# Kernel tuning notes

Measured on AMD Instinct MI355X. Metric: run time of the kernel, lower is better.

## Reference

```python
import jax, jax.numpy as jnp
import numpy as np

N = 1_048_576   # collocation points
D_IN = 3        # seq_net[0]
H = 32          # hidden width (seq_net[1..3])
B = 4           # seq_net[-1] = number of parallel branches / outputs


def setup_inputs() -> dict:
    key = jax.random.key(0)
    ks = jax.random.split(key, 9)

    def init_w(k, shape, fan_in):
        bound = 1.0 / np.sqrt(fan_in)
        return jax.random.uniform(k, shape, jnp.float32, -bound, bound)

    x = jax.random.normal(ks[0], (N, D_IN), dtype=jnp.float32)
    # Per-branch weights stacked on leading branch axis B (torch.nn.Linear init ranges).
    W0 = init_w(ks[1], (B, D_IN, H), D_IN)
    b0 = init_w(ks[2], (B, H), D_IN)
    W1 = init_w(ks[3], (B, H, H), H)
    b1 = init_w(ks[4], (B, H), H)
    W2 = init_w(ks[5], (B, H, H), H)
    b2 = init_w(ks[6], (B, H), H)
    W3 = init_w(ks[7], (B, H, 1), H)
    b3 = init_w(ks[8], (B, 1), H)
    return {"x": x, "W0": W0, "b0": b0, "W1": W1, "b1": b1,
            "W2": W2, "b2": b2, "W3": W3, "b3": b3}


def reference(x, W0, b0, W1, b1, W2, b2, W3, b3):
    # All B branches computed as one batched GEMM chain (same math as the
    # python loop over per-branch Linear+tanh stacks in PFNN.forward).
    h = jnp.tanh(jnp.einsum('nd,bdh->bnh', x, W0) + b0[:, None, :])   # [B,N,H]
    h = jnp.tanh(jnp.einsum('bnd,bdh->bnh', h, W1) + b1[:, None, :])  # [B,N,H]
    h = jnp.tanh(jnp.einsum('bnd,bdh->bnh', h, W2) + b2[:, None, :])  # [B,N,H]
    out = jnp.einsum('bnd,bdh->bnh', h, W3) + b3[:, None, :]          # [B,N,1]
    # torch.cat(preds, dim=1): branch outputs side by side -> [N, B]
    return jnp.transpose(out[:, :, 0])
```

## Files before the change

### kernel.cpp

```cpp
#include <hip/hip_runtime.h>


#define NPTS 1048576
#define BLOCK 256
#define HROW 80
#define SCALE 2.8853900817779268f

#define OFF_BSC  16384
#define OFF_W0F  17408
#define OFF_B0P  25600
#define OFF_W3P  26112

using f16   = _Float16;
using f16x8 = __attribute__((ext_vector_type(8))) _Float16;
using f32x4 = __attribute__((ext_vector_type(4))) float;
using hfx2  = decltype(__builtin_amdgcn_cvt_pkrtz(0.0f, 0.0f));

__device__ __forceinline__ void inv4c(float v0, float v1, float v2, float v3,
                                      float& o0, float& o1, float& o2, float& o3)
{
    float a0 = __builtin_amdgcn_exp2f(v0) + 1.0f;
    float a1 = __builtin_amdgcn_exp2f(v1) + 1.0f;
    float a2 = __builtin_amdgcn_exp2f(v2) + 1.0f;
    float a3 = __builtin_amdgcn_exp2f(v3) + 1.0f;
    float p01 = a0 * a1;
    float p23 = a2 * a3;
    float p   = p01 * p23;
    float r   = __builtin_amdgcn_rcpf(p);
    float r01 = r * p23;
    float r23 = r * p01;
    o0 = __builtin_fmaf(r01, a1, -0.5f);
    o1 = __builtin_fmaf(r01, a0, -0.5f);
    o2 = __builtin_fmaf(r23, a3, -0.5f);
    o3 = __builtin_fmaf(r23, a2, -0.5f);
}

__device__ __forceinline__ void epi_mt(const f32x4& c0, const f32x4& c1, int mt,
                                       unsigned char* __restrict__ H,
                                       int col, int quad)
{
    #pragma unroll
    for (int r = 0; r < 4; r += 2) {
        int p = mt * 16 + quad * 4 + r;
        float o0, o1, o2, o3;
        inv4c(c0[r], c1[r], c0[r + 1], c1[r + 1], o0, o1, o2, o3);
        union { hfx2 h; unsigned int u; } cv0, cv1;
        cv0.h = __builtin_amdgcn_cvt_pkrtz(o0, o1);
        cv1.h = __builtin_amdgcn_cvt_pkrtz(o2, o3);
        *reinterpret_cast<unsigned int*>(H + p * HROW + 4 * col)       = cv0.u;
        *reinterpret_cast<unsigned int*>(H + (p + 1) * HROW + 4 * col) = cv1.u;
    }
}

__global__ void prep_kernel(const float* __restrict__ W0, const float* __restrict__ b0,
                            const float* __restrict__ W1, const float* __restrict__ b1,
                            const float* __restrict__ W2, const float* __restrict__ b2,
                            const float* __restrict__ W3,
                            unsigned char* __restrict__ ws)
{
    int i = blockIdx.x * 256 + threadIdx.x;
    if (i < 8192) {
        int k = i & 31, n = (i >> 5) & 15, t = (i >> 9) & 1, b = (i >> 10) & 3, l = i >> 12;
        int f = 2 * n + t;
        const float* W = l ? W2 : W1;
        reinterpret_cast<f16*>(ws)[i] = (f16)(-2.0f * SCALE * W[(b * 32 + k) * 32 + f]);
    } else if (i < 8448) {
        int j = i - 8192;
        int n = j & 15, t = (j >> 4) & 1, b = (j >> 5) & 3, l = j >> 7;
        const float* bb = l ? b2 : b1;
        reinterpret_cast<float*>(ws + OFF_BSC)[(((l * 4 + b) * 16 + n) << 1) | t]
            = SCALE * bb[b * 32 + 2 * n + t];
    } else if (i < 12544) {
        int j = i - 8448;
        int k = j & 31, n = (j >> 5) & 15, t = (j >> 9) & 1, b = (j >> 10) & 3;
        int f = 2 * n + t;
        int q = k >> 3, jj = k & 7;
        int row = -1; bool lo = false;
        if (q == 0 && jj < 6)      row = (jj < 3) ? jj : jj - 3;
        else if (q == 1 && jj < 3) { row = jj; lo = true; }
        f16 outv = (f16)0.0f;
        if (row >= 0) {
            float w  = SCALE * W0[(b * 3 + row) * 32 + f];
            f16   wh = (f16)w;
            outv = lo ? (f16)(w - (float)wh) : wh;
        }
        reinterpret_cast<f16*>(ws + OFF_W0F)[((b * 2 + t) * 16 + n) * 32 + k] = outv;
    } else if (i < 12672) {
        int j = i - 12544;
        int n = j & 15, t = (j >> 4) & 1, b = j >> 5;
        reinterpret_cast<float*>(ws + OFF_B0P)[(((b) * 16 + n) << 1) | t]
            = SCALE * b0[b * 32 + 2 * n + t];
    } else if (i < 12736) {
        int j = i - 12672;
        union { hfx2 h; unsigned int u; } cv;
        cv.h = __builtin_amdgcn_cvt_pkrtz(-2.0f * W3[2 * j], -2.0f * W3[2 * j + 1]);
        reinterpret_cast<unsigned int*>(ws + OFF_W3P)[j] = cv.u;
    }
}

__global__ __launch_bounds__(BLOCK, 8) void pfnn_kernel(
    const float* __restrict__ x, const unsigned char* __restrict__ ws,
    const float* __restrict__ b3,
    float* __restrict__ out)
{
    __shared__ __align__(16) unsigned char Hl[4][64 * HROW];

    const f16*   Wf  = reinterpret_cast<const f16*>(ws);
    const float* Bsc = reinterpret_cast<const float*>(ws + OFF_BSC);
    const f16*   W0f = reinterpret_cast<const f16*>(ws + OFF_W0F);
    const float* B0p = reinterpret_cast<const float*>(ws + OFF_B0P);
    const unsigned int* W3p = reinterpret_cast<const unsigned int*>(ws + OFF_W3P);

    const int t    = threadIdx.x;
    const int lane = t & 63;
    const int wv   = t >> 6;
    const int col  = lane & 15;
    const int quad = lane >> 4;
    unsigned char* __restrict__ H = &Hl[wv][0];

    const int n0 = blockIdx.x * BLOCK + t;
    const float x0 = x[3 * n0 + 0];
    const float x1 = x[3 * n0 + 1];
    const float x2 = x[3 * n0 + 2];

    f16x8 xfrag[4];
    {
        union { hfx2 h; int u; } q0_, q1_, q2_;
        q0_.h = __builtin_amdgcn_cvt_pkrtz(x0, x1);
        float r0 = x0 - (float)q0_.h[0];
        float r1 = x1 - (float)q0_.h[1];
        q1_.h = __builtin_amdgcn_cvt_pkrtz(x2, r0);
        float r2 = x2 - (float)q1_.h[0];
        q2_.h = __builtin_amdgcn_cvt_pkrtz(r1, r2);
        int d0 = q0_.u, d1 = q1_.u, d2 = q2_.u;
        #pragma unroll
        for (int mt = 0; mt < 4; ++mt) {
            int addr = 4 * (mt * 16 + col);
            union { int i[4]; f16x8 f; } u;
            u.i[0] = __builtin_amdgcn_ds_bpermute(addr, d0);
            u.i[1] = __builtin_amdgcn_ds_bpermute(addr, d1);
            u.i[2] = __builtin_amdgcn_ds_bpermute(addr, d2);
            u.i[3] = 0;
            xfrag[mt] = u.f;
        }
    }

    float res[4];

    #pragma unroll 2
    for (int b = 0; b < 4; ++b) {
        {
            const f16* wb = W0f + (b * 2) * 512;
            f16x8 bf0 = *reinterpret_cast<const f16x8*>(wb + col * 32 + quad * 8);
            f16x8 bf1 = *reinterpret_cast<const f16x8*>(wb + 512 + col * 32 + quad * 8);
            const float2 bp = *reinterpret_cast<const float2*>(B0p + ((b * 16 + col) << 1));
            f32x4 ci0 = {bp.x, bp.x, bp.x, bp.x};
            f32x4 ci1 = {bp.y, bp.y, bp.y, bp.y};

            #pragma unroll
            for (int mt = 0; mt < 4; ++mt) {
                f32x4 c0 = __builtin_amdgcn_mfma_f32_16x16x32_f16(xfrag[mt], bf0, ci0, 0, 0, 0);
                f32x4 c1 = __builtin_amdgcn_mfma_f32_16x16x32_f16(xfrag[mt], bf1, ci1, 0, 0, 0);
                epi_mt(c0, c1, mt, H, col, quad);
            }
        }

        #pragma unroll
        for (int l = 0; l < 2; ++l) {
            const f16* wb = Wf + ((l * 4 + b) * 2) * 512;
            f16x8 bf0 = *reinterpret_cast<const f16x8*>(wb + col * 32 + quad * 8);
            f16x8 bf1 = *reinterpret_cast<const f16x8*>(wb + 512 + col * 32 + quad * 8);
            const float2 bp = *reinterpret_cast<const float2*>(
                Bsc + (((l * 4 + b) * 16 + col) << 1));
            f32x4 ci0 = {bp.x, bp.x, bp.x, bp.x};
            f32x4 ci1 = {bp.y, bp.y, bp.y, bp.y};

            #pragma unroll
            for (int mt = 0; mt < 4; ++mt) {
                const f16x8 av = *reinterpret_cast<const f16x8*>(
                    H + (mt * 16 + col) * HROW + quad * 16);
                f32x4 c0 = __builtin_amdgcn_mfma_f32_16x16x32_f16(av, bf0, ci0, 0, 0, 0);
                f32x4 c1 = __builtin_amdgcn_mfma_f32_16x16x32_f16(av, bf1, ci1, 0, 0, 0);
                epi_mt(c0, c1, mt, H, col, quad);
            }
        }

        {
            float o = b3[b];
            const unsigned char* row = H + lane * HROW;
            const unsigned int* w3p = W3p + b * 16;
            #pragma unroll
            for (int i = 0; i < 4; ++i) {
                uint4 u = *reinterpret_cast<const uint4*>(row + 16 * i);
#if __has_builtin(__builtin_amdgcn_fdot2)
                union { unsigned int uu; hfx2 hh; } h0, h1, h2, h3, w0, w1, w2, w3u;
                h0.uu = u.x; h1.uu = u.y; h2.uu = u.z; h3.uu = u.w;
                w0.uu = w3p[4 * i];     w1.uu = w3p[4 * i + 1];
                w2.uu = w3p[4 * i + 2]; w3u.uu = w3p[4 * i + 3];
                o = __builtin_amdgcn_fdot2(h0.hh, w0.hh, o, false);
                o = __builtin_amdgcn_fdot2(h1.hh, w1.hh, o, false);
                o = __builtin_amdgcn_fdot2(h2.hh, w2.hh, o, false);
                o = __builtin_amdgcn_fdot2(h3.hh, w3u.hh, o, false);
#else
                union { unsigned int uu; f16 h[2]; } hh[4], wwu[4];
                hh[0].uu = u.x; hh[1].uu = u.y; hh[2].uu = u.z; hh[3].uu = u.w;
                #pragma unroll
                for (int q = 0; q < 4; ++q) {
                    wwu[q].uu = w3p[4 * i + q];
                    o = __builtin_fmaf((float)hh[q].h[0], (float)wwu[q].h[0], o);
                    o = __builtin_fmaf((float)hh[q].h[1], (float)wwu[q].h[1], o);
                }
#endif
            }
            res[b] = o;
        }
    }

    float4 r4 = make_float4(res[0], res[1], res[2], res[3]);
    *reinterpret_cast<float4*>(out + 4 * n0) = r4;
}

extern "C" void kernel_launch(void* const* d_in, const int* in_sizes, int n_in,
                              void* d_out, int out_size, void* d_ws, size_t ws_size,
                              hipStream_t stream) {
    const float* x  = (const float*)d_in[0];
    const float* W0 = (const float*)d_in[1];
    const float* b0 = (const float*)d_in[2];
    const float* W1 = (const float*)d_in[3];
    const float* b1 = (const float*)d_in[4];
    const float* W2 = (const float*)d_in[5];
    const float* b2 = (const float*)d_in[6];
    const float* W3 = (const float*)d_in[7];
    const float* b3 = (const float*)d_in[8];
    float* out = (float*)d_out;
    unsigned char* ws = (unsigned char*)d_ws;

    prep_kernel<<<dim3(50), dim3(256), 0, stream>>>(W0, b0, W1, b1, W2, b2, W3, ws);
    pfnn_kernel<<<dim3(NPTS / BLOCK), dim3(BLOCK), 0, stream>>>(x, ws, b3, out);
}
```

Measured before the change: 161.6 us.

## Software-pipeline branch loop: overlap next layer0 with final dot product

Restructures the per-branch loop so the last layer's H rows are read into registers, then the next branch's first-layer MFMA runs before the final dot products are computed. The dot product is split into four independent accumulators so it is less serialized. The loop is no longer unrolled, which is meant to cut code size and register pressure. The tradeoff is that holding the H rows live across layer0 costs extra registers, and the changed summation order alters rounding slightly.

```diff
diff --git a/kernel.cpp b/kernel.cpp
--- a/kernel.cpp
+++ b/kernel.cpp
@@ -50,6 +50,76 @@
         *reinterpret_cast<unsigned int*>(H + p * HROW + 4 * col)       = cv0.u;
         *reinterpret_cast<unsigned int*>(H + (p + 1) * HROW + 4 * col) = cv1.u;
     }
+}
+
+__device__ __forceinline__ void layer0_block(int b, const f16x8 (&xfrag)[4],
+                                             const f16* __restrict__ W0f,
+                                             const float* __restrict__ B0p,
+                                             unsigned char* __restrict__ H,
+                                             int col, int quad)
+{
+    const f16* wb = W0f + (b * 2) * 512;
+    f16x8 bf0 = *reinterpret_cast<const f16x8*>(wb + col * 32 + quad * 8);
+    f16x8 bf1 = *reinterpret_cast<const f16x8*>(wb + 512 + col * 32 + quad * 8);
+    const float2 bp = *reinterpret_cast<const float2*>(B0p + ((b * 16 + col) << 1));
+    f32x4 ci0 = {bp.x, bp.x, bp.x, bp.x};
+    f32x4 ci1 = {bp.y, bp.y, bp.y, bp.y};
+
+    #pragma unroll
+    for (int mt = 0; mt < 4; ++mt) {
+        f32x4 c0 = __builtin_amdgcn_mfma_f32_16x16x32_f16(xfrag[mt], bf0, ci0, 0, 0, 0);
+        f32x4 c1 = __builtin_amdgcn_mfma_f32_16x16x32_f16(xfrag[mt], bf1, ci1, 0, 0, 0);
+        epi_mt(c0, c1, mt, H, col, quad);
+    }
+}
+
+__device__ __forceinline__ void hidden_block(int l, int b,
+                                             const f16* __restrict__ Wf,
+                                             const float* __restrict__ Bsc,
+                                             unsigned char* __restrict__ H,
+                                             int col, int quad)
+{
+    const f16* wb = Wf + ((l * 4 + b) * 2) * 512;
+    f16x8 bf0 = *reinterpret_cast<const f16x8*>(wb + col * 32 + quad * 8);
+    f16x8 bf1 = *reinterpret_cast<const f16x8*>(wb + 512 + col * 32 + quad * 8);
+    const float2 bp = *reinterpret_cast<const float2*>(
+        Bsc + (((l * 4 + b) * 16 + col) << 1));
+    f32x4 ci0 = {bp.x, bp.x, bp.x, bp.x};
+    f32x4 ci1 = {bp.y, bp.y, bp.y, bp.y};
+
+    #pragma unroll
+    for (int mt = 0; mt < 4; ++mt) {
+        const f16x8 av = *reinterpret_cast<const f16x8*>(
+            H + (mt * 16 + col) * HROW + quad * 16);
+        f32x4 c0 = __builtin_amdgcn_mfma_f32_16x16x32_f16(av, bf0, ci0, 0, 0, 0);
+        f32x4 c1 = __builtin_amdgcn_mfma_f32_16x16x32_f16(av, bf1, ci1, 0, 0, 0);
+        epi_mt(c0, c1, mt, H, col, quad);
+    }
+}
+
+__device__ __forceinline__ float dot8(unsigned int ux, unsigned int uy,
+                                      unsigned int uz, unsigned int uw,
+                                      uint4 w, float acc)
+{
+#if __has_builtin(__builtin_amdgcn_fdot2)
+    union { unsigned int uu; hfx2 hh; } a0, a1, a2, a3, b0, b1, b2, b3;
+    a0.uu = ux; a1.uu = uy; a2.uu = uz; a3.uu = uw;
+    b0.uu = w.x; b1.uu = w.y; b2.uu = w.z; b3.uu = w.w;
+    acc = __builtin_amdgcn_fdot2(a0.hh, b0.hh, acc, false);
+    acc = __builtin_amdgcn_fdot2(a1.hh, b1.hh, acc, false);
+    acc = __builtin_amdgcn_fdot2(a2.hh, b2.hh, acc, false);
+    acc = __builtin_amdgcn_fdot2(a3.hh, b3.hh, acc, false);
+#else
+    union { unsigned int uu; f16 h[2]; } a[4], bw[4];
+    a[0].uu = ux; a[1].uu = uy; a[2].uu = uz; a[3].uu = uw;
+    bw[0].uu = w.x; bw[1].uu = w.y; bw[2].uu = w.z; bw[3].uu = w.w;
+    #pragma unroll
+    for (int q = 0; q < 4; ++q) {
+        acc = __builtin_fmaf((float)a[q].h[0], (float)bw[q].h[0], acc);
+        acc = __builtin_fmaf((float)a[q].h[1], (float)bw[q].h[1], acc);
+    }
+#endif
+    return acc;
 }
 
 __global__ void prep_kernel(const float* __restrict__ W0, const float* __restrict__ b0,
@@ -146,74 +216,45 @@
     }
 
     float res[4];
-
-    #pragma unroll 2
-    for (int b = 0; b < 4; ++b) {
-        {
-            const f16* wb = W0f + (b * 2) * 512;
-            f16x8 bf0 = *reinterpret_cast<const f16x8*>(wb + col * 32 + quad * 8);
-            f16x8 bf1 = *reinterpret_cast<const f16x8*>(wb + 512 + col * 32 + quad * 8);
-            const float2 bp = *reinterpret_cast<const float2*>(B0p + ((b * 16 + col) << 1));
-            f32x4 ci0 = {bp.x, bp.x, bp.x, bp.x};
-            f32x4 ci1 = {bp.y, bp.y, bp.y, bp.y};
-
-            #pragma unroll
-            for (int mt = 0; mt < 4; ++mt) {
-                f32x4 c0 = __builtin_amdgcn_mfma_f32_16x16x32_f16(xfrag[mt], bf0, ci0, 0, 0, 0);
-                f32x4 c1 = __builtin_amdgcn_mfma_f32_16x16x32_f16(xfrag[mt], bf1, ci1, 0, 0, 0);
-                epi_mt(c0, c1, mt, H, col, quad);
-            }
-        }
-
-        #pragma unroll
-        for (int l = 0; l < 2; ++l) {
-            const f16* wb = Wf + ((l * 4 + b) * 2) * 512;
-            f16x8 bf0 = *reinterpret_cast<const f16x8*>(wb + col * 32 + quad * 8);
-            f16x8 bf1 = *reinterpret_cast<const f16x8*>(wb + 512 + col * 32 + quad * 8);
-            const float2 bp = *reinterpret_cast<const float2*>(
-                Bsc + (((l * 4 + b) * 16 + col) << 1));
-            f32x4 ci0 = {bp.x, bp.x, bp.x, bp.x};
-            f32x4 ci1 = {bp.y, bp.y, bp.y, bp.y};
-
-            #pragma unroll
-            for (int mt = 0; mt < 4; ++mt) {
-                const f16x8 av = *reinterpret_cast<const f16x8*>(
-                    H + (mt * 16 + col) * HROW + quad * 16);
-                f32x4 c0 = __builtin_amdgcn_mfma_f32_16x16x32_f16(av, bf0, ci0, 0, 0, 0);
-                f32x4 c1 = __builtin_amdgcn_mfma_f32_16x16x32_f16(av, bf1, ci1, 0, 0, 0);
-                epi_mt(c0, c1, mt, H, col, quad);
-            }
-        }
-
-        {
-            float o = b3[b];
-            const unsigned char* row = H + lane * HROW;
-            const unsigned int* w3p = W3p + b * 16;
-            #pragma unroll
-            for (int i = 0; i < 4; ++i) {
-                uint4 u = *reinterpret_cast<const uint4*>(row + 16 * i);
-#if __has_builtin(__builtin_amdgcn_fdot2)
-                union { unsigned int uu; hfx2 hh; } h0, h1, h2, h3, w0, w1, w2, w3u;
-                h0.uu = u.x; h1.uu = u.y; h2.uu = u.z; h3.uu = u.w;
-                w0.uu = w3p[4 * i];     w1.uu = w3p[4 * i + 1];
-                w2.uu = w3p[4 * i + 2]; w3u.uu = w3p[4 * i + 3];
-                o = __builtin_amdgcn_fdot2(h0.hh, w0.hh, o, false);
-                o = __builtin_amdgcn_fdot2(h1.hh, w1.hh, o, false);
-                o = __builtin_amdgcn_fdot2(h2.hh, w2.hh, o, false);
-                o = __builtin_amdgcn_fdot2(h3.hh, w3u.hh, o, false);
-#else
-                union { unsigned int uu; f16 h[2]; } hh[4], wwu[4];
-                hh[0].uu = u.x; hh[1].uu = u.y; hh[2].uu = u.z; hh[3].uu = u.w;
-                #pragma unroll
-                for (int q = 0; q < 4; ++q) {
-                    wwu[q].uu = w3p[4 * i + q];
-                    o = __builtin_fmaf((float)hh[q].h[0], (float)wwu[q].h[0], o);
-                    o = __builtin_fmaf((float)hh[q].h[1], (float)wwu[q].h[1], o);
-                }
-#endif
-            }
-            res[b] = o;
-        }
+    const unsigned char* __restrict__ row = H + lane * HROW;
+
+    layer0_block(0, xfrag, W0f, B0p, H, col, quad);
+
+    #pragma unroll 1
+    for (int b = 0; b < 3; ++b) {
+        hidden_block(0, b, Wf, Bsc, H, col, quad);
+        hidden_block(1, b, Wf, Bsc, H, col, quad);
+
+        uint4 u0 = *reinterpret_cast<const uint4*>(row);
+        uint4 u1 = *reinterpret_cast<const uint4*>(row + 16);
+        uint4 u2 = *reinterpret_cast<const uint4*>(row + 32);
+        uint4 u3 = *reinterpret_cast<const uint4*>(row + 48);
+
+        layer0_block(b + 1, xfrag, W0f, B0p, H, col, quad);
+
+        const uint4* wv4 = reinterpret_cast<const uint4*>(W3p + b * 16);
+        uint4 w0 = wv4[0], w1 = wv4[1], w2 = wv4[2], w3v = wv4[3];
+        float a0 = dot8(u0.x, u0.y, u0.z, u0.w, w0, b3[b]);
+        float a1 = dot8(u1.x, u1.y, u1.z, u1.w, w1, 0.0f);
+        float a2 = dot8(u2.x, u2.y, u2.z, u2.w, w2, 0.0f);
+        float a3 = dot8(u3.x, u3.y, u3.z, u3.w, w3v, 0.0f);
+        res[b] = (a0 + a1) + (a2 + a3);
+    }
+
+    {
+        hidden_block(0, 3, Wf, Bsc, H, col, quad);
+        hidden_block(1, 3, Wf, Bsc, H, col, quad);
+        uint4 u0 = *reinterpret_cast<const uint4*>(row);
+        uint4 u1 = *reinterpret_cast<const uint4*>(row + 16);
+        uint4 u2 = *reinterpret_cast<const uint4*>(row + 32);
+        uint4 u3 = *reinterpret_cast<const uint4*>(row + 48);
+        const uint4* wv4 = reinterpret_cast<const uint4*>(W3p + 3 * 16);
+        uint4 w0 = wv4[0], w1 = wv4[1], w2 = wv4[2], w3v = wv4[3];
+        float a0 = dot8(u0.x, u0.y, u0.z, u0.w, w0, b3[3]);
+        float a1 = dot8(u1.x, u1.y, u1.z, u1.w, w1, 0.0f);
+        float a2 = dot8(u2.x, u2.y, u2.z, u2.w, w2, 0.0f);
+        float a3 = dot8(u3.x, u3.y, u3.z, u3.w, w3v, 0.0f);
+        res[3] = (a0 + a1) + (a2 + a3);
     }
 
     float4 r4 = make_float4(res[0], res[1], res[2], res[3]);
```

Result: no change. 164.0 us (+1.5%).
